# Optimization experiments

Hardware: AMD Instinct MI355X
Metric: run time of the kernel (lower is better)

## Reference

```python
import jax, jax.numpy as jnp
import numpy as np

B, S, D = 1, 2048, 2048
H, KV, HD = 16, 8, 128
GROUP = H // KV
INTER = 6144
L = 2
VOCAB = 32000
EPS = 1e-6
THETA = 10000.0


def _rope_tables(seq_len, head_dim, theta):
    inv_freq = 1.0 / theta ** (np.arange(0, head_dim, 2, dtype=np.float32) / head_dim)
    pos = np.arange(seq_len, dtype=np.float32)
    ang = pos[:, None] * inv_freq[None, :]
    ang = np.concatenate([ang, ang], axis=1)  # [S, HD]
    return jnp.asarray(np.cos(ang)), jnp.asarray(np.sin(ang))


def setup_inputs() -> dict:
    key = jax.random.key(0)
    ks = jax.random.split(key, 16)
    sd = 0.02
    inp = {}
    inp['input_ids'] = jax.random.randint(ks[0], (B, S), 0, VOCAB, dtype=jnp.int32)
    inp['mask'] = jnp.triu(jnp.ones((S, S), dtype=bool), k=1)  # True = masked (future)
    cos, sin = _rope_tables(S, HD, THETA)
    inp['cos'], inp['sin'] = cos, sin
    inp['embed'] = jax.random.normal(ks[1], (VOCAB, D), jnp.float32) * sd
    # torch Linear convention: weight [out, in], y = x @ W.T
    inp['q_w'] = jax.random.normal(ks[2], (L, H * HD, D), jnp.float32) * sd
    inp['k_w'] = jax.random.normal(ks[3], (L, KV * HD, D), jnp.float32) * sd
    inp['v_w'] = jax.random.normal(ks[4], (L, KV * HD, D), jnp.float32) * sd
    inp['o_w'] = jax.random.normal(ks[5], (L, D, H * HD), jnp.float32) * sd
    inp['qn_scale'] = jnp.ones((L, HD), jnp.float32)
    inp['kn_scale'] = jnp.ones((L, HD), jnp.float32)
    inp['ln1_scale'] = jnp.ones((L, D), jnp.float32)
    inp['ln2_scale'] = jnp.ones((L, D), jnp.float32)
    inp['gate_w'] = jax.random.normal(ks[6], (L, INTER, D), jnp.float32) * sd
    inp['up_w'] = jax.random.normal(ks[7], (L, INTER, D), jnp.float32) * sd
    inp['down_w'] = jax.random.normal(ks[8], (L, D, INTER), jnp.float32) * sd
    return inp


def rms_norm(x, scale, eps=EPS):
    xf = x.astype(jnp.float32)
    var = jnp.mean(xf * xf, axis=-1, keepdims=True)
    return (xf * jax.lax.rsqrt(var + eps) * scale).astype(x.dtype)


def apply_rope(x, cos, sin):
    # x: [B, heads, S, HD]
    s = x.shape[2]
    hd = x.shape[-1]
    x1, x2 = x[..., : hd // 2], x[..., hd // 2:]
    rotated = jnp.concatenate([-x2, x1], axis=-1)
    return x * cos[None, None, :s] + rotated * sin[None, None, :s]


def decoder_layer(h, p, mask, cos, sin):
    (q_w, k_w, v_w, o_w, qn, kn, ln1, ln2, gate_w, up_w, down_w) = p
    b, s, _ = h.shape
    x = rms_norm(h, ln1)
    q = (x @ q_w.T).reshape(b, s, H, HD).transpose(0, 2, 1, 3)   # [B,H,S,HD]
    k = (x @ k_w.T).reshape(b, s, KV, HD).transpose(0, 2, 1, 3)  # [B,KV,S,HD]
    v = (x @ v_w.T).reshape(b, s, KV, HD).transpose(0, 2, 1, 3)
    q = rms_norm(q, qn)
    k = rms_norm(k, kn)
    q = apply_rope(q, cos, sin)
    k = apply_rope(k, cos, sin)
    kr = jnp.repeat(k, GROUP, axis=1)  # GQA head expansion
    vr = jnp.repeat(v, GROUP, axis=1)
    scores = jnp.einsum('bhqd,bhkd->bhqk', q, kr) / jnp.sqrt(jnp.float32(HD))
    scores = jnp.where(mask[None, None], -jnp.inf, scores)
    attn = jax.nn.softmax(scores, axis=-1)
    ctx = jnp.einsum('bhqk,bhkd->bhqd', attn, vr)
    ctx = ctx.transpose(0, 2, 1, 3).reshape(b, s, H * HD)
    h = h + ctx @ o_w.T
    x = rms_norm(h, ln2)
    mlp = (jax.nn.silu(x @ gate_w.T) * (x @ up_w.T)) @ down_w.T
    return h + mlp


def reference(input_ids, mask, cos, sin, embed, q_w, k_w, v_w, o_w,
              qn_scale, kn_scale, ln1_scale, ln2_scale, gate_w, up_w, down_w):
    h = embed[input_ids]  # [B, S, D]
    params = (q_w, k_w, v_w, o_w, qn_scale, kn_scale, ln1_scale, ln2_scale,
              gate_w, up_w, down_w)

    def body(carry, p):
        return decoder_layer(carry, p, mask, cos, sin), None

    h, _ = jax.lax.scan(body, h, params)
    return h
```

## Files before the change

### kernel.cpp

```cpp
#include <hip/hip_runtime.h>
#include <hip/hip_bf16.h>

static constexpr int SEQ   = 2048;
static constexpr int DM    = 2048;
static constexpr int NHEAD = 16;
static constexpr int NKVH  = 8;
static constexpr int HDIM  = 128;
static constexpr int FFN   = 6144;
static constexpr int NLAYER = 2;
static constexpr float EPSV = 1e-6f;
static constexpr int QKVN  = NHEAD * HDIM + 2 * NKVH * HDIM;

typedef __attribute__((ext_vector_type(8))) short bf16x8;
typedef __attribute__((ext_vector_type(4))) float f32x4;

__device__ __forceinline__ float wave_sum(float v) {
#pragma unroll
    for (int o = 32; o > 0; o >>= 1) v += __shfl_xor(v, o);
    return v;
}

__device__ __forceinline__ void gload16(const void* g, void* l) {
    __builtin_amdgcn_global_load_lds(
        (const __attribute__((address_space(1))) void*)g,
        (__attribute__((address_space(3))) void*)l,
        16, 0, 0);
}

__global__ void embed_k(const int* __restrict__ ids, const float* __restrict__ emb,
                        float* __restrict__ h) {
    const int s = blockIdx.x;
    const long src = (long)ids[s] * DM;
    for (int t = threadIdx.x; t < DM; t += 256)
        h[(long)s * DM + t] = emb[src + t];
}

__global__ void rmsnorm_k(const float* __restrict__ in, const float* __restrict__ g,
                          __hip_bfloat16* __restrict__ out) {
    const int row = blockIdx.x;
    const float* r = in + (long)row * DM;
    const int tid = threadIdx.x;
    float v[8];
    float ss = 0.f;
#pragma unroll
    for (int t = 0; t < 8; ++t) { v[t] = r[tid + t * 256]; ss += v[t] * v[t]; }
    ss = wave_sum(ss);
    __shared__ float sp[4];
    if ((tid & 63) == 0) sp[tid >> 6] = ss;
    __syncthreads();
    ss = sp[0] + sp[1] + sp[2] + sp[3];
    const float inv = rsqrtf(ss * (1.f / DM) + EPSV);
    __hip_bfloat16* o_ = out + (long)row * DM;
#pragma unroll
    for (int t = 0; t < 8; ++t) {
        const int j = tid + t * 256;
        o_[j] = __float2bfloat16(v[t] * inv * g[j]);
    }
}

__global__ void rmsnorm_res4_k(const __hip_bfloat16* __restrict__ part, long n,
                               float* __restrict__ h, const float* __restrict__ g,
                               __hip_bfloat16* __restrict__ x) {
    const int row = blockIdx.x;
    const int tid = threadIdx.x;
    const long base = (long)row * DM + tid * 8;
    float v[8];
    *(float4*)&v[0] = *(const float4*)(h + base);
    *(float4*)&v[4] = *(const float4*)(h + base + 4);
#pragma unroll
    for (int z = 0; z < 4; ++z) {
        union { bf16x8 vv; __hip_bfloat16 e[8]; } p;
        p.vv = *(const bf16x8*)(part + (long)z * n + base);
#pragma unroll
        for (int j = 0; j < 8; ++j) v[j] += __bfloat162float(p.e[j]);
    }
    *(float4*)(h + base) = *(float4*)&v[0];
    *(float4*)(h + base + 4) = *(float4*)&v[4];
    float ss = 0.f;
#pragma unroll
    for (int j = 0; j < 8; ++j) ss += v[j] * v[j];
    ss = wave_sum(ss);
    __shared__ float sp[4];
    if ((tid & 63) == 0) sp[tid >> 6] = ss;
    __syncthreads();
    ss = sp[0] + sp[1] + sp[2] + sp[3];
    const float inv = rsqrtf(ss * (1.f / DM) + EPSV);
    const float4 g0 = *(const float4*)(g + tid * 8);
    const float4 g1 = *(const float4*)(g + tid * 8 + 4);
    union { bf16x8 vv; __hip_bfloat16 e[8]; } o;
    o.e[0] = __float2bfloat16(v[0] * inv * g0.x); o.e[1] = __float2bfloat16(v[1] * inv * g0.y);
    o.e[2] = __float2bfloat16(v[2] * inv * g0.z); o.e[3] = __float2bfloat16(v[3] * inv * g0.w);
    o.e[4] = __float2bfloat16(v[4] * inv * g1.x); o.e[5] = __float2bfloat16(v[5] * inv * g1.y);
    o.e[6] = __float2bfloat16(v[6] * inv * g1.z); o.e[7] = __float2bfloat16(v[7] * inv * g1.w);
    *(bf16x8*)(x + base) = o.vv;
}

__global__ void red4res_k(const __hip_bfloat16* __restrict__ p, long n, float* __restrict__ h) {
    const long i = ((long)blockIdx.x * 256 + threadIdx.x) * 8;
    float v[8];
    *(float4*)&v[0] = *(const float4*)(h + i);
    *(float4*)&v[4] = *(const float4*)(h + i + 4);
#pragma unroll
    for (int z = 0; z < 4; ++z) {
        union { bf16x8 vv; __hip_bfloat16 e[8]; } b;
        b.vv = *(const bf16x8*)(p + (long)z * n + i);
#pragma unroll
        for (int j = 0; j < 8; ++j) v[j] += __bfloat162float(b.e[j]);
    }
    *(float4*)(h + i) = *(float4*)&v[0];
    *(float4*)(h + i + 4) = *(float4*)&v[4];
}

__global__ void qknorm_rope_k(const __hip_bfloat16* __restrict__ in, long zStride, int inOff,
                              const float* __restrict__ ns,
                              const float* __restrict__ cosT, const float* __restrict__ sinT,
                              __hip_bfloat16* __restrict__ out, int nheads) {
    const int idx = blockIdx.x * 4 + (threadIdx.x >> 6);
    const int lane = threadIdx.x & 63;
    const int s = idx / nheads;
    const int hh = idx - s * nheads;
    const long base = (long)s * QKVN + inOff + hh * HDIM;
    const float x1 = __bfloat162float(in[base + lane]) + __bfloat162float(in[zStride + base + lane]);
    const float x2 = __bfloat162float(in[base + lane + 64]) + __bfloat162float(in[zStride + base + lane + 64]);
    float ss = wave_sum(x1 * x1 + x2 * x2);
    const float inv = rsqrtf(ss * (1.f / HDIM) + EPSV);
    const float n1 = x1 * inv * ns[lane];
    const float n2 = x2 * inv * ns[lane + 64];
    const float c1 = cosT[s * HDIM + lane],      c2 = cosT[s * HDIM + 64 + lane];
    const float s1 = sinT[s * HDIM + lane],      s2 = sinT[s * HDIM + 64 + lane];
    __hip_bfloat16* w = out + ((long)hh * SEQ + s) * HDIM;
    w[lane]      = __float2bfloat16(n1 * c1 - n2 * s1);
    w[lane + 64] = __float2bfloat16(n2 * c2 + n1 * s2);
}

__global__ void vtrans_k(const __hip_bfloat16* __restrict__ vf, long zStride, int colOff,
                         __hip_bfloat16* __restrict__ vt) {
    __shared__ float tile[64][65];
    const int s0 = blockIdx.x * 64, d0 = blockIdx.y * 64, kv = blockIdx.z;
    const int lane = threadIdx.x & 63, part = threadIdx.x >> 6;
    for (int r = part; r < 64; r += 4) {
        const long idx = (long)(s0 + r) * QKVN + colOff + kv * HDIM + d0 + lane;
        tile[r][lane] = __bfloat162float(vf[idx]) + __bfloat162float(vf[zStride + idx]);
    }
    __syncthreads();
    for (int r = part; r < 64; r += 4)
        vt[((long)kv * HDIM + d0 + r) * SEQ + s0 + lane] = __float2bfloat16(tile[lane][r]);
}

__global__ void silu_red2_k(const __hip_bfloat16* __restrict__ p, long n,
                            __hip_bfloat16* __restrict__ out) {
    const long i = ((long)blockIdx.x * 256 + threadIdx.x) * 8;
    union { bf16x8 v; __hip_bfloat16 e[8]; } g0, g1, u0, u1, o;
    g0.v = *(const bf16x8*)(p + i);
    g1.v = *(const bf16x8*)(p + n + i);
    u0.v = *(const bf16x8*)(p + 2 * n + i);
    u1.v = *(const bf16x8*)(p + 3 * n + i);
#pragma unroll
    for (int j = 0; j < 8; ++j) {
        const float g = __bfloat162float(g0.e[j]) + __bfloat162float(g1.e[j]);
        const float u = __bfloat162float(u0.e[j]) + __bfloat162float(u1.e[j]);
        const float sv = g / (1.f + __expf(-g));
        o.e[j] = __float2bfloat16(sv * u);
    }
    *(bf16x8*)(out + i) = o.v;
}

__global__ __launch_bounds__(256)
void flash_k(const __hip_bfloat16* __restrict__ qb, const __hip_bfloat16* __restrict__ kb,
             const __hip_bfloat16* __restrict__ vt, __hip_bfloat16* __restrict__ ctx) {
    __shared__ __align__(16) char ks[2][16384];
    __shared__ __align__(16) char vs[2][16384];
    __shared__ __align__(16) char ps[4][2048];

    const int tid = threadIdx.x;
    const int lane = tid & 63;
    const int wid = tid >> 6;
    const int l15 = lane & 15;
    const int l4 = lane >> 4;

    const int h = blockIdx.y;
    const int kvh = h >> 1;
    const float scale = 0.0883883476483184405f;

    auto stageK = [&](int buf, int kt) {
        const __hip_bfloat16* kg = kb + ((long)kvh * SEQ + kt * 64) * HDIM;
#pragma unroll
        for (int i = 0; i < 4; ++i) {
            const int c = i * 256 + tid;
            const int r = c >> 4, s = c & 15;
            gload16(kg + (long)r * HDIM + ((s ^ (r & 7)) * 8), ks[buf] + c * 16);
        }
    };
    auto stageV = [&](int buf, int kt) {
        const __hip_bfloat16* vg = vt + (long)kvh * HDIM * SEQ + kt * 64;
#pragma unroll
        for (int i = 0; i < 4; ++i) {
            const int c = i * 256 + tid;
            const int r = c >> 3, s = c & 7;
            gload16(vg + (long)r * SEQ + ((s ^ (r & 7)) * 8), vs[buf] + c * 16);
        }
    };

#pragma unroll
    for (int half = 0; half < 2; ++half) {
        const int x = half ? 31 - blockIdx.x : blockIdx.x;
        const int q0 = x * 64;
        const int nkt = x + 1;

        bf16x8 aq[4];
        {
            const __hip_bfloat16* qg = qb + ((long)h * SEQ + q0 + wid * 16 + l15) * HDIM + l4 * 8;
#pragma unroll
            for (int kk = 0; kk < 4; ++kk) aq[kk] = *(const bf16x8*)(qg + kk * 32);
        }

        float mreg[4], lreg[4];
#pragma unroll
        for (int j = 0; j < 4; ++j) { mreg[j] = -3.0e38f; lreg[j] = 0.f; }
        f32x4 oacc[8];
#pragma unroll
        for (int n = 0; n < 8; ++n) oacc[n] = (f32x4){0.f, 0.f, 0.f, 0.f};

        stageK(0, 0); stageV(0, 0);
        asm volatile("s_waitcnt vmcnt(0)" ::: "memory");
        __builtin_amdgcn_s_barrier();

        for (int kt = 0; kt < nkt; ++kt) {
            const int cur = kt & 1;
            if (kt + 1 < nkt) { stageK(cur ^ 1, kt + 1); stageV(cur ^ 1, kt + 1); }

            f32x4 sac[4];
#pragma unroll
            for (int n = 0; n < 4; ++n) sac[n] = (f32x4){0.f, 0.f, 0.f, 0.f};
            __builtin_amdgcn_s_setprio(1);
#pragma unroll
            for (int kk = 0; kk < 4; ++kk) {
#pragma unroll
                for (int n = 0; n < 4; ++n) {
                    const int r = n * 16 + l15;
                    const bf16x8 bk = *(const bf16x8*)(ks[cur] + r * 256 + (((kk * 4 + l4) ^ (r & 7)) << 4));
                    sac[n] = __builtin_amdgcn_mfma_f32_16x16x32_bf16(aq[kk], bk, sac[n], 0, 0, 0);
                }
            }
            __builtin_amdgcn_s_setprio(0);

            const bool diag = (kt + 1 == nkt);
            float mnj[4], alj[4];
#pragma unroll
            for (int j = 0; j < 4; ++j) {
                float mx = -3.0e38f;
#pragma unroll
                for (int n = 0; n < 4; ++n) {
                    float v = sac[n][j] * scale;
                    if (diag && (n * 16 + l15 > wid * 16 + l4 * 4 + j)) v = -3.0e38f;
                    sac[n][j] = v;
                    mx = fmaxf(mx, v);
                }
#pragma unroll
                for (int o = 1; o < 16; o <<= 1) mx = fmaxf(mx, __shfl_xor(mx, o));
                const float mn = fmaxf(mreg[j], mx);
                mnj[j] = mn;
                alj[j] = __expf(mreg[j] - mn);
                mreg[j] = mn;
            }
#pragma unroll
            for (int j = 0; j < 4; ++j) {
                float rs = 0.f;
#pragma unroll
                for (int n = 0; n < 4; ++n) {
                    const float e = __expf(sac[n][j] - mnj[j]);
                    sac[n][j] = e;
                    rs += e;
                }
#pragma unroll
                for (int o = 1; o < 16; o <<= 1) rs += __shfl_xor(rs, o);
                lreg[j] = lreg[j] * alj[j] + rs;
#pragma unroll
                for (int n2 = 0; n2 < 8; ++n2) oacc[n2][j] *= alj[j];
            }

            char* pw = ps[wid];
#pragma unroll
            for (int n = 0; n < 4; ++n)
#pragma unroll
                for (int j = 0; j < 4; ++j) {
                    const int r = l4 * 4 + j;
                    const int col = n * 16 + l15;
                    *(__hip_bfloat16*)(pw + r * 128 + (((col >> 3) ^ (r & 7)) << 4) + (col & 7) * 2) =
                        __float2bfloat16(sac[n][j]);
                }
            asm volatile("s_waitcnt lgkmcnt(0)" ::: "memory");
            __builtin_amdgcn_sched_barrier(0);
            __builtin_amdgcn_s_setprio(1);
#pragma unroll
            for (int kk = 0; kk < 2; ++kk) {
                const bf16x8 ap = *(const bf16x8*)(pw + l15 * 128 + (((kk * 4 + l4) ^ (l15 & 7)) << 4));
#pragma unroll
                for (int n2 = 0; n2 < 8; ++n2) {
                    const int r = n2 * 16 + l15;
                    const bf16x8 bv = *(const bf16x8*)(vs[cur] + r * 128 + (((kk * 4 + l4) ^ (r & 7)) << 4));
                    oacc[n2] = __builtin_amdgcn_mfma_f32_16x16x32_bf16(ap, bv, oacc[n2], 0, 0, 0);
                }
            }
            __builtin_amdgcn_s_setprio(0);

            asm volatile("s_waitcnt vmcnt(0)" ::: "memory");
            __builtin_amdgcn_s_barrier();
        }

#pragma unroll
        for (int j = 0; j < 4; ++j) {
            const float inv = 1.f / lreg[j];
            const long rowb = (long)(q0 + wid * 16 + l4 * 4 + j) * (NHEAD * HDIM) + h * HDIM;
#pragma unroll
            for (int n2 = 0; n2 < 8; ++n2)
                ctx[rowb + n2 * 16 + l15] = __float2bfloat16(oacc[n2][j] * inv);
        }
    }
}

template <int ZSEL>
__global__ __launch_bounds__(512, 2)
void g8p(const __hip_bfloat16* __restrict__ A,
         const float* __restrict__ Ba, const float* __restrict__ Bb, const float* __restrict__ Bc,
         __hip_bfloat16* __restrict__ C, int kLen, int ldA, int ldB, int ldC,
         int seg1, int seg2, long cZStride, int kZStride, int zDiv) {
    __shared__ __align__(16) char sA[2][2][16384];
    __shared__ __align__(16) char sB[2][2][16384];

    const int tid = threadIdx.x;
    const int lane = tid & 63;
    const int wid = tid >> 6;
    const int wr = wid >> 2;
    const int wc = wid & 3;
    const int l15 = lane & 15;
    const int l4 = lane >> 4;

    const int row0 = blockIdx.y * 256;
    const int col0 = blockIdx.x * 256;
    const int z = blockIdx.z;

    const float* B;
    int colB;
    if (ZSEL) {
        B = (z / zDiv) ? Bb : Ba; colB = col0;
    } else {
        if (col0 >= seg2)      { B = Bc; colB = col0 - seg2; }
        else if (col0 >= seg1) { B = Bb; colB = col0 - seg1; }
        else                   { B = Ba; colB = col0; }
    }
    const long cOff = (long)z * cZStride;
    const int k0z = (z % zDiv) * kZStride;
    const int nk = kLen / 64;

    f32x4 acc[8][4];
#pragma unroll
    for (int m = 0; m < 8; ++m)
#pragma unroll
        for (int n = 0; n < 4; ++n)
            acc[m][n] = (f32x4){0.f, 0.f, 0.f, 0.f};

    auto stageA = [&](int half, int kt) {
        const __hip_bfloat16* base = A + (long)(row0 + half * 128) * ldA;
        char* dst = sA[kt & 1][half];
        const int k0 = k0z + kt * 64;
#pragma unroll
        for (int i = 0; i < 2; ++i) {
            const int c = i * 512 + tid;
            const int r = c >> 3, s = c & 7;
            gload16(base + (long)r * ldA + k0 + ((s ^ (r & 7)) * 8), dst + c * 16);
        }
    };
    auto loadB = [&](float4* rb, int half, int kt) {
        const int k0 = k0z + kt * 64;
        const float* base = B + (long)(colB + half * 128) * ldB + k0;
#pragma unroll
        for (int i = 0; i < 2; ++i) {
            const int sidx = i * 512 + tid;
            const int r = sidx >> 3, q = sidx & 7;
            const float* p = base + (long)r * ldB + q * 8;
            rb[i * 2]     = *(const float4*)p;
            rb[i * 2 + 1] = *(const float4*)(p + 4);
        }
    };
    auto writeB = [&](const float4* rb, int half, int kt) {
        char* dst = sB[kt & 1][half];
#pragma unroll
        for (int i = 0; i < 2; ++i) {
            const int sidx = i * 512 + tid;
            const int r = sidx >> 3, q = sidx & 7;
            union { bf16x8 v; __hip_bfloat16 e[8]; } u;
            const float* f = (const float*)&rb[i * 2];
#pragma unroll
            for (int j = 0; j < 8; ++j) u.e[j] = __float2bfloat16(f[j]);
            *(bf16x8*)(dst + (r * 8 + (q ^ (r & 7))) * 16) = u.v;
        }
    };

    auto readA = [&](int buf, int p, int mm, int ks) -> bf16x8 {
        const int r = p * 32 + mm * 16 + l15;
        const int q = ks * 4 + l4;
        return *(const bf16x8*)(sA[buf][wr] + r * 128 + ((q ^ (r & 7)) << 4));
    };
    auto readB = [&](int buf, int nn, int ks) -> bf16x8 {
        const int r = (wc & 1) * 64 + nn * 16 + l15;
        const int q = ks * 4 + l4;
        return *(const bf16x8*)(sB[buf][wc >> 1] + r * 128 + ((q ^ (r & 7)) << 4));
    };

    float4 rb0[4], rb1[4];
    loadB(rb0, 0, 0);
    stageA(0, 0); stageA(1, 0);
    asm volatile("s_waitcnt vmcnt(4)" ::: "memory");
    writeB(rb0, 0, 0);
    loadB(rb1, 1, 0);
    asm volatile("s_waitcnt vmcnt(0)" ::: "memory");
    writeB(rb1, 1, 0);
    if (nk > 1) { loadB(rb0, 0, 1); loadB(rb1, 1, 1); }
    asm volatile("s_waitcnt lgkmcnt(0)" ::: "memory");
    __builtin_amdgcn_sched_barrier(0);
    __builtin_amdgcn_s_barrier();

    bf16x8 bfrag[4][2];
    for (int t = 0; t < nk; ++t) {
        const int cur = t & 1;
#pragma unroll
        for (int p = 0; p < 4; ++p) {
            bf16x8 a[2][2];
            a[0][0] = readA(cur, p, 0, 0); a[0][1] = readA(cur, p, 0, 1);
            a[1][0] = readA(cur, p, 1, 0); a[1][1] = readA(cur, p, 1, 1);
            if (p == 0) {
#pragma unroll
                for (int n = 0; n < 4; ++n) {
                    bfrag[n][0] = readB(cur, n, 0);
                    bfrag[n][1] = readB(cur, n, 1);
                }
            }
            if (p == 0 && t + 1 < nk) { stageA(0, t + 1); writeB(rb0, 0, t + 1); }
            if (p == 1 && t + 1 < nk) { stageA(1, t + 1); writeB(rb1, 1, t + 1); }
            if (p == 2 && t + 2 < nk) loadB(rb0, 0, t + 2);
            if (p == 3 && t + 2 < nk) loadB(rb1, 1, t + 2);

            if (p == 0) asm volatile("s_waitcnt lgkmcnt(8)" ::: "memory");
            __builtin_amdgcn_sched_barrier(0);
            if (p == 3) {
                if (t + 2 < nk)      asm volatile("s_waitcnt vmcnt(8)" ::: "memory");
                else if (t + 1 < nk) asm volatile("s_waitcnt vmcnt(0)" ::: "memory");
            }
            __builtin_amdgcn_s_barrier();
            asm volatile("s_waitcnt lgkmcnt(0)" ::: "memory");
            __builtin_amdgcn_sched_barrier(0);

            __builtin_amdgcn_s_setprio(1);
#pragma unroll
            for (int ks = 0; ks < 2; ++ks)
#pragma unroll
                for (int mm = 0; mm < 2; ++mm)
#pragma unroll
                    for (int n = 0; n < 4; ++n)
                        acc[p * 2 + mm][n] = __builtin_amdgcn_mfma_f32_16x16x32_bf16(
                            a[mm][ks], bfrag[n][ks], acc[p * 2 + mm][n], 0, 0, 0);
            __builtin_amdgcn_s_setprio(0);
            __builtin_amdgcn_sched_barrier(0);
            __builtin_amdgcn_s_barrier();
        }
    }

#pragma unroll
    for (int m = 0; m < 8; ++m) {
#pragma unroll
        for (int n = 0; n < 4; ++n) {
            const int rb = row0 + wr * 128 + m * 16 + l4 * 4;
            const int cc = col0 + wc * 64 + n * 16 + l15;
#pragma unroll
            for (int j = 0; j < 4; ++j)
                C[cOff + (long)(rb + j) * ldC + cc] = __float2bfloat16(acc[m][n][j]);
        }
    }
}

extern "C" void kernel_launch(void* const* d_in, const int* in_sizes, int n_in,
                              void* d_out, int out_size, void* d_ws, size_t ws_size,
                              hipStream_t stream) {
    const int*   ids  = (const int*)d_in[0];
    const float* cosT = (const float*)d_in[2];
    const float* sinT = (const float*)d_in[3];
    const float* emb  = (const float*)d_in[4];
    const float* q_w  = (const float*)d_in[5];
    const float* k_w  = (const float*)d_in[6];
    const float* v_w  = (const float*)d_in[7];
    const float* o_w  = (const float*)d_in[8];
    const float* qn   = (const float*)d_in[9];
    const float* kn   = (const float*)d_in[10];
    const float* ln1  = (const float*)d_in[11];
    const float* ln2  = (const float*)d_in[12];
    const float* gw   = (const float*)d_in[13];
    const float* uw   = (const float*)d_in[14];
    const float* dw   = (const float*)d_in[15];

    char* W = (char*)d_ws;
    size_t off = 0;
    auto take = [&](size_t nb) { char* p = W + off; off += (nb + 255) & ~(size_t)255; return p; };

    float*          h    = (float*)          take((size_t)SEQ * DM * 4);
    __hip_bfloat16* x    = (__hip_bfloat16*) take((size_t)SEQ * DM * 2);
    __hip_bfloat16* part = (__hip_bfloat16*) take((size_t)4 * SEQ * FFN * 2);
    __hip_bfloat16* qb   = (__hip_bfloat16*) take((size_t)NHEAD * SEQ * HDIM * 2);
    __hip_bfloat16* kb   = (__hip_bfloat16*) take((size_t)NKVH * SEQ * HDIM * 2);
    __hip_bfloat16* vt   = (__hip_bfloat16*) take((size_t)NKVH * HDIM * SEQ * 2);
    __hip_bfloat16* ctx  = (__hip_bfloat16*) take((size_t)SEQ * NHEAD * HDIM * 2);
    __hip_bfloat16* go   = (__hip_bfloat16*) take((size_t)SEQ * FFN * 2);
    if (off > ws_size) return;

    embed_k<<<SEQ, 256, 0, stream>>>(ids, emb, h);
    rmsnorm_k<<<SEQ, 256, 0, stream>>>(h, ln1, x);

    const long nQKV = (long)SEQ * QKVN;
    const long nDM  = (long)SEQ * DM;
    const long nFFN = (long)SEQ * FFN;
    const int BIG = 1 << 30;

    for (int l = 0; l < NLAYER; ++l) {
        const float* qwl = q_w + (size_t)l * (NHEAD * HDIM) * DM;
        const float* kwl = k_w + (size_t)l * (NKVH * HDIM) * DM;
        const float* vwl = v_w + (size_t)l * (NKVH * HDIM) * DM;
        const float* owl = o_w + (size_t)l * DM * (NHEAD * HDIM);
        const float* gwl = gw  + (size_t)l * FFN * DM;
        const float* uwl = uw  + (size_t)l * FFN * DM;
        const float* dwl = dw  + (size_t)l * DM * FFN;

        g8p<0><<<dim3(QKVN / 256, SEQ / 256, 2), 512, 0, stream>>>(
            x, qwl, kwl, vwl, part, DM / 2, DM, DM, QKVN,
            NHEAD * HDIM, NHEAD * HDIM + NKVH * HDIM, nQKV, DM / 2, 2);

        qknorm_rope_k<<<SEQ * NHEAD / 4, 256, 0, stream>>>(
            part, nQKV, 0, qn + l * HDIM, cosT, sinT, qb, NHEAD);
        qknorm_rope_k<<<SEQ * NKVH / 4, 256, 0, stream>>>(
            part, nQKV, NHEAD * HDIM, kn + l * HDIM, cosT, sinT, kb, NKVH);
        vtrans_k<<<dim3(SEQ / 64, HDIM / 64, NKVH), 256, 0, stream>>>(
            part, nQKV, NHEAD * HDIM + NKVH * HDIM, vt);

        flash_k<<<dim3(16, NHEAD), 256, 0, stream>>>(qb, kb, vt, ctx);

        g8p<0><<<dim3(DM / 256, SEQ / 256, 4), 512, 0, stream>>>(
            ctx, owl, owl, owl, part, (NHEAD * HDIM) / 4, NHEAD * HDIM, NHEAD * HDIM, DM,
            BIG, BIG, nDM, (NHEAD * HDIM) / 4, 4);
        rmsnorm_res4_k<<<SEQ, 256, 0, stream>>>(part, nDM, h, ln2 + l * DM, x);

        g8p<1><<<dim3(FFN / 256, SEQ / 256, 4), 512, 0, stream>>>(
            x, gwl, uwl, uwl, part, DM / 2, DM, DM, FFN,
            BIG, BIG, nFFN, DM / 2, 2);
        silu_red2_k<<<(int)(nFFN / 2048), 256, 0, stream>>>(part, nFFN, go);

        g8p<0><<<dim3(DM / 256, SEQ / 256, 4), 512, 0, stream>>>(
            go, dwl, dwl, dwl, part, FFN / 4, FFN, FFN, DM,
            BIG, BIG, nDM, FFN / 4, 4);
        if (l + 1 < NLAYER)
            rmsnorm_res4_k<<<SEQ, 256, 0, stream>>>(part, nDM, h, ln1 + (l + 1) * DM, x);
        else
            red4res_k<<<(int)(nDM / 2048), 256, 0, stream>>>(part, nDM, h);
    }

    hipMemcpyAsync(d_out, h, (size_t)out_size * sizeof(float), hipMemcpyDeviceToDevice, stream);
}
```

Measured before the change: 847.9 us.

## Merge GEMM k-loop into two phases per tile to halve barriers

Restructures the GEMM main loop so each K-tile runs as two phases of two A sub-blocks each, instead of four phases of one. This halves the number of s_barrier syncs per tile and issues larger MFMA bursts. It also regroups the LDS writes and global prefetches into those two phases. The cost is more live A-fragment registers, and the shifted waitcnt placement changes how much load latency is overlapped.

```diff
diff --git a/kernel.cpp b/kernel.cpp
--- a/kernel.cpp
+++ b/kernel.cpp
@@ -424,42 +424,84 @@
     bf16x8 bfrag[4][2];
     for (int t = 0; t < nk; ++t) {
         const int cur = t & 1;
-#pragma unroll
-        for (int p = 0; p < 4; ++p) {
-            bf16x8 a[2][2];
-            a[0][0] = readA(cur, p, 0, 0); a[0][1] = readA(cur, p, 0, 1);
-            a[1][0] = readA(cur, p, 1, 0); a[1][1] = readA(cur, p, 1, 1);
-            if (p == 0) {
-#pragma unroll
-                for (int n = 0; n < 4; ++n) {
-                    bfrag[n][0] = readB(cur, n, 0);
-                    bfrag[n][1] = readB(cur, n, 1);
-                }
-            }
-            if (p == 0 && t + 1 < nk) { stageA(0, t + 1); writeB(rb0, 0, t + 1); }
-            if (p == 1 && t + 1 < nk) { stageA(1, t + 1); writeB(rb1, 1, t + 1); }
-            if (p == 2 && t + 2 < nk) loadB(rb0, 0, t + 2);
-            if (p == 3 && t + 2 < nk) loadB(rb1, 1, t + 2);
-
-            if (p == 0) asm volatile("s_waitcnt lgkmcnt(8)" ::: "memory");
+
+        {
+            bf16x8 a0[2][2], a1[2][2];
+            a0[0][0] = readA(cur, 0, 0, 0); a0[0][1] = readA(cur, 0, 0, 1);
+            a0[1][0] = readA(cur, 0, 1, 0); a0[1][1] = readA(cur, 0, 1, 1);
+            a1[0][0] = readA(cur, 1, 0, 0); a1[0][1] = readA(cur, 1, 0, 1);
+            a1[1][0] = readA(cur, 1, 1, 0); a1[1][1] = readA(cur, 1, 1, 1);
+#pragma unroll
+            for (int n = 0; n < 4; ++n) {
+                bfrag[n][0] = readB(cur, n, 0);
+                bfrag[n][1] = readB(cur, n, 1);
+            }
+            if (t + 1 < nk) {
+                writeB(rb0, 0, t + 1);
+                writeB(rb1, 1, t + 1);
+                stageA(0, t + 1);
+                stageA(1, t + 1);
+            }
+            asm volatile("s_waitcnt lgkmcnt(8)" ::: "memory");
             __builtin_amdgcn_sched_barrier(0);
-            if (p == 3) {
-                if (t + 2 < nk)      asm volatile("s_waitcnt vmcnt(8)" ::: "memory");
-                else if (t + 1 < nk) asm volatile("s_waitcnt vmcnt(0)" ::: "memory");
-            }
             __builtin_amdgcn_s_barrier();
             asm volatile("s_waitcnt lgkmcnt(0)" ::: "memory");
             __builtin_amdgcn_sched_barrier(0);
 
             __builtin_amdgcn_s_setprio(1);
 #pragma unroll
-            for (int ks = 0; ks < 2; ++ks)
+            for (int ks = 0; ks < 2; ++ks) {
 #pragma unroll
                 for (int mm = 0; mm < 2; ++mm)
 #pragma unroll
                     for (int n = 0; n < 4; ++n)
-                        acc[p * 2 + mm][n] = __builtin_amdgcn_mfma_f32_16x16x32_bf16(
-                            a[mm][ks], bfrag[n][ks], acc[p * 2 + mm][n], 0, 0, 0);
+                        acc[mm][n] = __builtin_amdgcn_mfma_f32_16x16x32_bf16(
+                            a0[mm][ks], bfrag[n][ks], acc[mm][n], 0, 0, 0);
+#pragma unroll
+                for (int mm = 0; mm < 2; ++mm)
+#pragma unroll
+                    for (int n = 0; n < 4; ++n)
+                        acc[2 + mm][n] = __builtin_amdgcn_mfma_f32_16x16x32_bf16(
+                            a1[mm][ks], bfrag[n][ks], acc[2 + mm][n], 0, 0, 0);
+            }
+            __builtin_amdgcn_s_setprio(0);
+            __builtin_amdgcn_sched_barrier(0);
+            __builtin_amdgcn_s_barrier();
+        }
+
+        {
+            bf16x8 a2[2][2], a3[2][2];
+            a2[0][0] = readA(cur, 2, 0, 0); a2[0][1] = readA(cur, 2, 0, 1);
+            a2[1][0] = readA(cur, 2, 1, 0); a2[1][1] = readA(cur, 2, 1, 1);
+            a3[0][0] = readA(cur, 3, 0, 0); a3[0][1] = readA(cur, 3, 0, 1);
+            a3[1][0] = readA(cur, 3, 1, 0); a3[1][1] = readA(cur, 3, 1, 1);
+            if (t + 2 < nk) {
+                loadB(rb0, 0, t + 2);
+                loadB(rb1, 1, t + 2);
+            }
+            __builtin_amdgcn_sched_barrier(0);
+            if (t + 2 < nk)      asm volatile("s_waitcnt vmcnt(8)" ::: "memory");
+            else if (t + 1 < nk) asm volatile("s_waitcnt vmcnt(0)" ::: "memory");
+            __builtin_amdgcn_s_barrier();
+            asm volatile("s_waitcnt lgkmcnt(0)" ::: "memory");
+            __builtin_amdgcn_sched_barrier(0);
+
+            __builtin_amdgcn_s_setprio(1);
+#pragma unroll
+            for (int ks = 0; ks < 2; ++ks) {
+#pragma unroll
+                for (int mm = 0; mm < 2; ++mm)
+#pragma unroll
+                    for (int n = 0; n < 4; ++n)
+                        acc[4 + mm][n] = __builtin_amdgcn_mfma_f32_16x16x32_bf16(
+                            a2[mm][ks], bfrag[n][ks], acc[4 + mm][n], 0, 0, 0);
+#pragma unroll
+                for (int mm = 0; mm < 2; ++mm)
+#pragma unroll
+                    for (int n = 0; n < 4; ++n)
+                        acc[6 + mm][n] = __builtin_amdgcn_mfma_f32_16x16x32_bf16(
+                            a3[mm][ks], bfrag[n][ks], acc[6 + mm][n], 0, 0, 0);
+            }
             __builtin_amdgcn_s_setprio(0);
             __builtin_amdgcn_sched_barrier(0);
             __builtin_amdgcn_s_barrier();
```

Result: no change. 842.7 us (-0.6%).
